# Kernel tuning notes

Measured on AMD Instinct MI355X. Metric: run time of the kernel, lower is better.

Reference implementation:

```python
import jax, jax.numpy as jnp
import numpy as np

B, L, E, H = 2, 2048, 1024, 16
HD = E // H          # head_dim = 64
G = H // 4           # heads per kernel-size group = 4


def _dwconv(x, w, b):
    """Causal depthwise conv. x: (B, G, L, D); w: (D, k); b: (D,).
    Matches PadLeft(k-1) + Conv1d(D, D, k, groups=D): y[l] = sum_j w[:, j] * x[l - (k-1) + j] + b."""
    k = w.shape[-1]
    Lx = x.shape[2]
    xp = jnp.pad(x, ((0, 0), (0, 0), (k - 1, 0), (0, 0)))
    out = b
    for j in range(k):
        out = out + xp[:, :, j:j + Lx, :] * w[:, j]
    return out


def setup_inputs() -> dict:
    key = jax.random.key(0)
    ks = jax.random.split(key, 32)
    s = 0.02
    inp = {"x": jax.random.normal(ks[0], (B, L, E), jnp.float32)}
    for i, n in enumerate(["Wq", "Wk", "Wv", "Wo"]):
        inp[n] = jax.random.normal(ks[1 + i], (E, E), jnp.float32) * s
    inp["bo"] = jax.random.normal(ks[5], (E,), jnp.float32) * s
    i = 6
    for ksz in (3, 5, 7):
        for pfx in ("q", "k", "v"):
            inp[f"{pfx}{ksz}_w"] = jax.random.normal(ks[i], (HD, ksz), jnp.float32) * (1.0 / ksz)
            inp[f"{pfx}{ksz}_b"] = jax.random.normal(ks[i + 1], (HD,), jnp.float32) * s
            i += 2
    return inp


def reference(x, Wq, Wk, Wv, Wo, bo,
              q3_w, q3_b, k3_w, k3_b, v3_w, v3_b,
              q5_w, q5_b, k5_w, k5_b, v5_w, v5_b,
              q7_w, q7_b, k7_w, k7_b, v7_w, v7_b):
    b, l, _ = x.shape

    def split(t):  # (b, l, E) -> (b, 4, G, l, HD)
        return t.reshape(b, l, 4, G, HD).transpose(0, 2, 3, 1, 4)

    q = split(x @ Wq.T)
    k = split(x @ Wk.T)
    v = split(x @ Wv.T)

    # NOTE: faithful to source quirks -- k and v convs are applied to the
    # (already convolved) q group, not to k/v.
    q0, k0, v0 = q[:, 0], k[:, 0], v[:, 0]
    q1 = _dwconv(q[:, 1], q3_w, q3_b)
    k1 = _dwconv(q1, k3_w, k3_b)
    v1 = _dwconv(q1, v3_w, v3_b)
    q2 = _dwconv(q[:, 2], q5_w, q5_b)
    k2 = _dwconv(q2, k5_w, k5_b)
    v2 = _dwconv(q2, v5_w, v5_b)
    q3 = _dwconv(q[:, 3], q7_w, q7_b)
    k3 = _dwconv(q3, k7_w, k7_b)
    v3 = _dwconv(q3, v7_w, v7_b)

    Q = jnp.concatenate([q0, q1, q2, q3], axis=1)  # (b, H, l, HD)
    K = jnp.concatenate([k0, k1, k2, k3], axis=1)
    V = jnp.concatenate([v0, v1, v2, v3], axis=1)

    logit = jnp.einsum('bnid,bnjd->bnij', Q, K) * (HD ** -0.5)
    attn = jax.nn.softmax(logit, axis=-1)
    attn_out = jnp.einsum('bnij,bnjd->bnid', attn, V)

    # Source quirk: output uses rearranged V, discarding attn_out.
    out = V.transpose(0, 2, 1, 3).reshape(b, l, E)
    # keep the attention compute alive without changing the math
    out = out + 0.0 * attn_out.transpose(0, 2, 1, 3).reshape(b, l, E)
    return out @ Wo.T + bo
```

## Files before the change

kernel.cpp:

```cpp
#include <hip/hip_runtime.h>
#include <hip/hip_bf16.h>
#include <stdint.h>

#define L_SEQ 2048
#define MTOT  4096
#define EDIM  1024

typedef __attribute__((ext_vector_type(8))) short bf16x8;
typedef __attribute__((ext_vector_type(4))) float f32x4;
typedef __attribute__((ext_vector_type(4))) float float4v;
typedef __attribute__((ext_vector_type(4))) unsigned short us4;

__device__ __forceinline__ unsigned short f2b(float f) {
    union { float f; unsigned u; } v; v.f = f;
    return (unsigned short)((v.u + 0x7FFFu + ((v.u >> 16) & 1u)) >> 16);
}
__device__ __forceinline__ float b2f(unsigned short h) {
    union { unsigned u; float f; } v; v.u = ((unsigned)h) << 16;
    return v.f;
}
__device__ __forceinline__ unsigned cvtpk(float lo, float hi) {
    unsigned r;
    asm("v_cvt_pk_bf16_f32 %0, %1, %2" : "=v"(r) : "v"(lo), "v"(hi));
    return r;
}

__device__ __forceinline__ void lds16(const void* g, void* l) {
    __builtin_amdgcn_global_load_lds((const __attribute__((address_space(1))) void*)g,
                                     (__attribute__((address_space(3))) void*)l, 16, 0, 0);
}

__global__ __launch_bounds__(256) void wprep_kernel(
    const float* __restrict__ Wq, const float* __restrict__ Wv,
    const float* __restrict__ Wo,
    unsigned short* __restrict__ W1b, unsigned short* __restrict__ Wob,
    const float* __restrict__ q3w, const float* __restrict__ q3b,
    const float* __restrict__ v3w, const float* __restrict__ v3b,
    const float* __restrict__ q5w, const float* __restrict__ q5b,
    const float* __restrict__ v5w, const float* __restrict__ v5b,
    const float* __restrict__ q7w, const float* __restrict__ q7b,
    const float* __restrict__ v7w, const float* __restrict__ v7b,
    float* __restrict__ H, float* __restrict__ Beff, float* __restrict__ Corr)
{
    if (blockIdx.x >= 2048) {
        int ch = (blockIdx.x - 2048) * 256 + threadIdx.x;
        int g = ch >> 8;
        int d = ch & 63;
        int k = 3 + 2 * g;
        const float* qw = (g == 0) ? q3w : (g == 1) ? q5w : q7w;
        const float* qb = (g == 0) ? q3b : (g == 1) ? q5b : q7b;
        const float* vw = (g == 0) ? v3w : (g == 1) ? v5w : v7w;
        const float* vb = (g == 0) ? v3b : (g == 1) ? v5b : v7b;

        float hq[7], hv[7];
        for (int i = 0; i < 7; ++i) { hq[i] = 0.f; hv[i] = 0.f; }
        for (int i = 0; i < k; ++i) {
            hq[i] = qw[d * k + (k - 1 - i)];
            hv[i] = vw[d * k + (k - 1 - i)];
        }
        float h[13];
        for (int i = 0; i < 13; ++i) h[i] = 0.f;
        for (int a = 0; a < 7; ++a)
            for (int b = 0; b < 7; ++b)
                h[a + b] += hq[a] * hv[b];
        for (int i = 0; i < 13; ++i) H[i * 768 + ch] = h[i];

        float sv = 0.f;
        for (int j = 0; j < k; ++j) sv += vw[d * k + j];
        Beff[ch] = qb[d] * sv + vb[d];

        for (int l = 0; l < 6; ++l) {
            float s2 = 0.f;
            for (int i = l + 1; i < 7; ++i) s2 += hv[i];
            Corr[l * 768 + ch] = qb[d] * s2;
        }
        return;
    }
    const int WQ = (EDIM * EDIM) / 4;
    int i = blockIdx.x * 256 + threadIdx.x;
    const float* src;
    unsigned short* dst;
    int j;
    if (i < WQ) {
        j = i * 4;
        int row = j >> 10;
        src = (row < 256) ? Wv : Wq;
        dst = W1b;
    } else {
        j = (i - WQ) * 4; src = Wo; dst = Wob;
    }
    float4v v = *(const float4v*)(src + j);
    us4 o;
    o[0] = f2b(v[0]); o[1] = f2b(v[1]); o[2] = f2b(v[2]); o[3] = f2b(v[3]);
    *(us4*)(dst + j) = o;
}

template <int TA, int OUT_MODE>
__global__ __launch_bounds__(512, 2) void gemm_f(
    const float* __restrict__ Af,
    const unsigned short* __restrict__ Ab0, const unsigned short* __restrict__ Ab1,
    int tsplit,
    const unsigned short* __restrict__ BT,
    unsigned short* __restrict__ Cb, float* __restrict__ Cf,
    const float* __restrict__ bias)
{
    constexpr int ABUF = TA ? 49152 : 32768;
    constexpr int ABYT = TA ? 32768 : 16384;
    __shared__ uint8_t sh[3 * ABUF];

    int orig = blockIdx.y * 8 + blockIdx.x;
    int wg   = (orig & 7) * 32 + (orig >> 3);
    const int m0 = (wg >> 3) * 128, n0 = (wg & 7) * 128;

    const int tid  = threadIdx.x;
    const int wid  = tid >> 6;
    const int lane = tid & 63;
    const int wr   = wid >> 2;
    const int wc   = (wid >> 1) & 1;
    const int kh   = wid & 1;
    const int fr   = lane & 15, fq = lane >> 4;

    f32x4 acc[4][4] = {};

    auto stage = [&](int buf, int t) {
        uint8_t* Abase = sh + buf * ABUF;
        uint8_t* Bbase = Abase + ABYT;
        if (TA) {
            const float* Asrc = Af + (size_t)m0 * EDIM + t * 64;
#pragma unroll
            for (int j = 0; j < 4; ++j) {
                int slot = j * 512 + tid;
                int row = slot >> 4, c = (slot & 15) ^ (row & 15);
                lds16(Asrc + (size_t)row * EDIM + c * 4,
                      Abase + j * 8192 + wid * 1024);
            }
        } else {
            const unsigned short* Asrc =
                (t < tsplit ? Ab0 : Ab1) + (size_t)m0 * EDIM + t * 64;
#pragma unroll
            for (int j = 0; j < 2; ++j) {
                int slot = j * 512 + tid;
                int row = slot >> 3, c = (slot & 7) ^ (row & 7);
                lds16(Asrc + (size_t)row * EDIM + c * 8,
                      Abase + j * 8192 + wid * 1024);
            }
        }
        const unsigned short* Bsrc = BT + (size_t)n0 * EDIM + t * 64;
#pragma unroll
        for (int j = 0; j < 2; ++j) {
            int slot = j * 512 + tid;
            int row = slot >> 3, c = (slot & 7) ^ (row & 7);
            lds16(Bsrc + (size_t)row * EDIM + c * 8,
                  Bbase + j * 8192 + wid * 1024);
        }
    };

    auto compute = [&](int buf) {
        const uint8_t* Abase = sh + buf * ABUF;
        const unsigned short* bs = (const unsigned short*)(Abase + ABYT);
        bf16x8 a[4], b[4];
#pragma unroll
        for (int mi = 0; mi < 4; ++mi) {
            int row = wr * 64 + mi * 16 + fr;
            if (TA) {
                const float* as = (const float*)Abase;
                int c0 = kh * 8 + fq * 2;
                f32x4 lo = *(const f32x4*)(as + row * 64 + ((c0 ^ (row & 15)) * 4));
                f32x4 hi = *(const f32x4*)(as + row * 64 + (((c0 + 1) ^ (row & 15)) * 4));
                union { unsigned u[4]; bf16x8 v; } fu;
                fu.u[0] = cvtpk(lo[0], lo[1]); fu.u[1] = cvtpk(lo[2], lo[3]);
                fu.u[2] = cvtpk(hi[0], hi[1]); fu.u[3] = cvtpk(hi[2], hi[3]);
                a[mi] = fu.v;
            } else {
                const unsigned short* as = (const unsigned short*)Abase;
                a[mi] = *(const bf16x8*)(as + row * 64 + (((kh * 4 + fq) ^ (row & 7)) * 8));
            }
        }
#pragma unroll
        for (int ni = 0; ni < 4; ++ni) {
            int row = wc * 64 + ni * 16 + fr;
            b[ni] = *(const bf16x8*)(bs + row * 64 + (((kh * 4 + fq) ^ (row & 7)) * 8));
        }
#pragma unroll
        for (int mi = 0; mi < 4; ++mi)
#pragma unroll
            for (int ni = 0; ni < 4; ++ni)
                acc[mi][ni] = __builtin_amdgcn_mfma_f32_16x16x32_bf16(a[mi], b[ni], acc[mi][ni], 0, 0, 0);
    };

    const int NT = EDIM >> 6;
    stage(0, 0);
    stage(1, 1);
    if (TA) asm volatile("s_waitcnt vmcnt(6)" ::: "memory");
    else    asm volatile("s_waitcnt vmcnt(4)" ::: "memory");
    __builtin_amdgcn_s_barrier();
    asm volatile("" ::: "memory");

    for (int t = 0; t < NT; ++t) {
        if (t + 2 < NT) stage((t + 2) % 3, t + 2);
        compute(t % 3);
        if (t + 1 < NT) {
            if (t + 2 < NT) {
                if (TA) asm volatile("s_waitcnt vmcnt(6)" ::: "memory");
                else    asm volatile("s_waitcnt vmcnt(4)" ::: "memory");
            } else {
                asm volatile("s_waitcnt vmcnt(0)" ::: "memory");
            }
            __builtin_amdgcn_s_barrier();
            asm volatile("" ::: "memory");
        }
    }

    __syncthreads();
    float* Mg = (float*)sh;
    const int mgbase = (wr * 2 + wc) * 4096;
    if (kh) {
#pragma unroll
        for (int mi = 0; mi < 4; ++mi)
#pragma unroll
            for (int ni = 0; ni < 4; ++ni) {
                int col = ni * 16 + fr;
                int adr = mgbase + col * 64 + (((mi * 4 + fq) ^ (col & 15)) << 2);
                *(f32x4*)(Mg + adr) = acc[mi][ni];
            }
    }
    __syncthreads();
    if (!kh) {
#pragma unroll
        for (int mi = 0; mi < 4; ++mi) {
#pragma unroll
            for (int ni = 0; ni < 4; ++ni) {
                int col = ni * 16 + fr;
                int adr = mgbase + col * 64 + (((mi * 4 + fq) ^ (col & 15)) << 2);
                f32x4 p = *(const f32x4*)(Mg + adr);
                int gcol = n0 + wc * 64 + col;
                int rowb = m0 + wr * 64 + mi * 16 + fq * 4;
#pragma unroll
                for (int j = 0; j < 4; ++j) {
                    float v = acc[mi][ni][j] + p[j];
                    if (OUT_MODE == 0) {
                        Cb[(size_t)(rowb + j) * EDIM + gcol] = f2b(v);
                    } else {
                        Cf[(size_t)(rowb + j) * EDIM + gcol] = v + bias[gcol];
                    }
                }
            }
        }
    }
}

__global__ __launch_bounds__(256) void conv_kernel(
    const unsigned short* __restrict__ T, unsigned short* __restrict__ V,
    const float* __restrict__ H, const float* __restrict__ Beff,
    const float* __restrict__ Corr)
{
    unsigned w  = blockIdx.x * 256 + threadIdx.x;
    unsigned rp = w / 192u;
    int c4 = (int)(w - rp * 192u);
    int m  = (int)rp * 2;
    int ch = c4 * 4;
    int e0 = 256 + ch;
    const unsigned short* tp = T + (size_t)m * EDIM + e0;
    unsigned short*       vp = V + (size_t)m * EDIM + e0;
    int l  = m & (L_SEQ - 1);
    float4v b4 = *(const float4v*)(Beff + ch);
    float4v acc0 = b4, acc1 = b4;

    {
        float4v h = *(const float4v*)(H + ch);
        us4 t = *(const us4*)(tp + EDIM);
        acc1[0] += h[0] * b2f(t[0]); acc1[1] += h[1] * b2f(t[1]);
        acc1[2] += h[2] * b2f(t[2]); acc1[3] += h[3] * b2f(t[3]);
    }
    int ni = (l < 12) ? l : 12;
    for (int i = 0; i <= ni; ++i) {
        us4 t = *(const us4*)(tp - (size_t)i * EDIM);
        float4v h0 = *(const float4v*)(H + i * 768 + ch);
        acc0[0] += h0[0] * b2f(t[0]); acc0[1] += h0[1] * b2f(t[1]);
        acc0[2] += h0[2] * b2f(t[2]); acc0[3] += h0[3] * b2f(t[3]);
        if (i < 12) {
            float4v h1 = *(const float4v*)(H + (i + 1) * 768 + ch);
            acc1[0] += h1[0] * b2f(t[0]); acc1[1] += h1[1] * b2f(t[1]);
            acc1[2] += h1[2] * b2f(t[2]); acc1[3] += h1[3] * b2f(t[3]);
        }
    }
    if (l < 6) {
        float4v c = *(const float4v*)(Corr + l * 768 + ch);
        acc0[0] -= c[0]; acc0[1] -= c[1]; acc0[2] -= c[2]; acc0[3] -= c[3];
    }
    if (l + 1 < 6) {
        float4v c = *(const float4v*)(Corr + (l + 1) * 768 + ch);
        acc1[0] -= c[0]; acc1[1] -= c[1]; acc1[2] -= c[2]; acc1[3] -= c[3];
    }
    us4 o0, o1;
    o0[0] = f2b(acc0[0]); o0[1] = f2b(acc0[1]); o0[2] = f2b(acc0[2]); o0[3] = f2b(acc0[3]);
    o1[0] = f2b(acc1[0]); o1[1] = f2b(acc1[1]); o1[2] = f2b(acc1[2]); o1[3] = f2b(acc1[3]);
    *(us4*)vp = o0;
    *(us4*)(vp + EDIM) = o1;
}

extern "C" void kernel_launch(void* const* d_in, const int* in_sizes, int n_in,
                              void* d_out, int out_size, void* d_ws, size_t ws_size,
                              hipStream_t stream)
{
    const float* x  = (const float*)d_in[0];
    const float* Wq = (const float*)d_in[1];
    const float* Wv = (const float*)d_in[3];
    const float* Wo = (const float*)d_in[4];
    const float* bo = (const float*)d_in[5];

    uint8_t* ws = (uint8_t*)d_ws;
    unsigned short* W1b = (unsigned short*)(ws);
    unsigned short* Wob = (unsigned short*)(ws + (2u  << 20));
    unsigned short* T   = (unsigned short*)(ws + (4u  << 20));
    unsigned short* V   = (unsigned short*)(ws + (12u << 20));
    float* H    = (float*)(ws + (20u << 20));
    float* Beff = (float*)(ws + (20u << 20) + (64u << 10));
    float* Corr = (float*)(ws + (20u << 20) + (96u << 10));

    wprep_kernel<<<2051, 256, 0, stream>>>(
        Wq, Wv, Wo, W1b, Wob,
        (const float*)d_in[6],  (const float*)d_in[7],
        (const float*)d_in[10], (const float*)d_in[11],
        (const float*)d_in[12], (const float*)d_in[13],
        (const float*)d_in[16], (const float*)d_in[17],
        (const float*)d_in[18], (const float*)d_in[19],
        (const float*)d_in[22], (const float*)d_in[23],
        H, Beff, Corr);

    dim3 gg(EDIM / 128, MTOT / 128);
    gemm_f<1, 0><<<gg, 512, 0, stream>>>(x, nullptr, nullptr, 0,
                                         W1b, T, nullptr, nullptr);

    conv_kernel<<<1536, 256, 0, stream>>>(T, V, H, Beff, Corr);

    gemm_f<0, 1><<<gg, 512, 0, stream>>>(nullptr, T, V, 4,
                                         Wob, nullptr, (float*)d_out, bo);
}
```

Before: 53.42 us.

## Fuse weight prep, two GEMMs and conv into one persistent kernel with grid barriers

Replaces four separate kernel launches with a single 256-block persistent kernel. It runs weight conversion, the first GEMM, the depthwise conv and the output GEMM in sequence, separated by a software grid barrier built from hierarchical atomic counters. The aim is to remove launch gaps and tail effects between stages. The risks are spin-wait barrier cost, a shared memory size fixed at the larger GEMM's needs (which can limit occupancy), an extra memset for the barrier state, and a dependence on all 256 blocks being co-resident.

New measurement: 147.3 us. 2.76x slower.

```diff
diff --git a/kernel.cpp b/kernel.cpp
--- a/kernel.cpp
+++ b/kernel.cpp
@@ -24,79 +24,42 @@
     asm("v_cvt_pk_bf16_f32 %0, %1, %2" : "=v"(r) : "v"(lo), "v"(hi));
     return r;
 }
-
 __device__ __forceinline__ void lds16(const void* g, void* l) {
     __builtin_amdgcn_global_load_lds((const __attribute__((address_space(1))) void*)g,
                                      (__attribute__((address_space(3))) void*)l, 16, 0, 0);
 }
 
-__global__ __launch_bounds__(256) void wprep_kernel(
-    const float* __restrict__ Wq, const float* __restrict__ Wv,
-    const float* __restrict__ Wo,
-    unsigned short* __restrict__ W1b, unsigned short* __restrict__ Wob,
-    const float* __restrict__ q3w, const float* __restrict__ q3b,
-    const float* __restrict__ v3w, const float* __restrict__ v3b,
-    const float* __restrict__ q5w, const float* __restrict__ q5b,
-    const float* __restrict__ v5w, const float* __restrict__ v5b,
-    const float* __restrict__ q7w, const float* __restrict__ q7b,
-    const float* __restrict__ v7w, const float* __restrict__ v7b,
-    float* __restrict__ H, float* __restrict__ Beff, float* __restrict__ Corr)
-{
-    if (blockIdx.x >= 2048) {
-        int ch = (blockIdx.x - 2048) * 256 + threadIdx.x;
-        int g = ch >> 8;
-        int d = ch & 63;
-        int k = 3 + 2 * g;
-        const float* qw = (g == 0) ? q3w : (g == 1) ? q5w : q7w;
-        const float* qb = (g == 0) ? q3b : (g == 1) ? q5b : q7b;
-        const float* vw = (g == 0) ? v3w : (g == 1) ? v5w : v7w;
-        const float* vb = (g == 0) ? v3b : (g == 1) ? v5b : v7b;
-
-        float hq[7], hv[7];
-        for (int i = 0; i < 7; ++i) { hq[i] = 0.f; hv[i] = 0.f; }
-        for (int i = 0; i < k; ++i) {
-            hq[i] = qw[d * k + (k - 1 - i)];
-            hv[i] = vw[d * k + (k - 1 - i)];
-        }
-        float h[13];
-        for (int i = 0; i < 13; ++i) h[i] = 0.f;
-        for (int a = 0; a < 7; ++a)
-            for (int b = 0; b < 7; ++b)
-                h[a + b] += hq[a] * hv[b];
-        for (int i = 0; i < 13; ++i) H[i * 768 + ch] = h[i];
-
-        float sv = 0.f;
-        for (int j = 0; j < k; ++j) sv += vw[d * k + j];
-        Beff[ch] = qb[d] * sv + vb[d];
-
-        for (int l = 0; l < 6; ++l) {
-            float s2 = 0.f;
-            for (int i = l + 1; i < 7; ++i) s2 += hv[i];
-            Corr[l * 768 + ch] = qb[d] * s2;
-        }
-        return;
-    }
-    const int WQ = (EDIM * EDIM) / 4;
-    int i = blockIdx.x * 256 + threadIdx.x;
-    const float* src;
-    unsigned short* dst;
-    int j;
-    if (i < WQ) {
-        j = i * 4;
-        int row = j >> 10;
-        src = (row < 256) ? Wv : Wq;
-        dst = W1b;
-    } else {
-        j = (i - WQ) * 4; src = Wo; dst = Wob;
-    }
-    float4v v = *(const float4v*)(src + j);
-    us4 o;
-    o[0] = f2b(v[0]); o[1] = f2b(v[1]); o[2] = f2b(v[2]); o[3] = f2b(v[3]);
-    *(us4*)(dst + j) = o;
+__device__ __forceinline__ void gridbar(unsigned* st) {
+    __syncthreads();
+    if (threadIdx.x == 0) {
+        __threadfence();
+        unsigned* gcnt = st + (blockIdx.x & 7) * 16;
+        unsigned* mid  = st + 128;
+        unsigned* gen  = st + 129;
+        unsigned g0 = __hip_atomic_load(gen, __ATOMIC_RELAXED, __HIP_MEMORY_SCOPE_AGENT);
+        unsigned a  = __hip_atomic_fetch_add(gcnt, 1u, __ATOMIC_ACQ_REL, __HIP_MEMORY_SCOPE_AGENT);
+        bool done = false;
+        if (a == 31u) {
+            unsigned m = __hip_atomic_fetch_add(mid, 1u, __ATOMIC_ACQ_REL, __HIP_MEMORY_SCOPE_AGENT);
+            if (m == 7u) {
+                for (int i = 0; i < 8; ++i)
+                    __hip_atomic_store(st + i * 16, 0u, __ATOMIC_RELAXED, __HIP_MEMORY_SCOPE_AGENT);
+                __hip_atomic_store(mid, 0u, __ATOMIC_RELAXED, __HIP_MEMORY_SCOPE_AGENT);
+                __hip_atomic_fetch_add(gen, 1u, __ATOMIC_RELEASE, __HIP_MEMORY_SCOPE_AGENT);
+                done = true;
+            }
+        }
+        if (!done) {
+            while (__hip_atomic_load(gen, __ATOMIC_ACQUIRE, __HIP_MEMORY_SCOPE_AGENT) == g0)
+                __builtin_amdgcn_s_sleep(4);
+        }
+    }
+    __syncthreads();
 }
 
 template <int TA, int OUT_MODE>
-__global__ __launch_bounds__(512, 2) void gemm_f(
+__device__ __forceinline__ void gemm_phase(
+    uint8_t* sh, int blk,
     const float* __restrict__ Af,
     const unsigned short* __restrict__ Ab0, const unsigned short* __restrict__ Ab1,
     int tsplit,
@@ -106,10 +69,8 @@
 {
     constexpr int ABUF = TA ? 49152 : 32768;
     constexpr int ABYT = TA ? 32768 : 16384;
-    __shared__ uint8_t sh[3 * ABUF];
-
-    int orig = blockIdx.y * 8 + blockIdx.x;
-    int wg   = (orig & 7) * 32 + (orig >> 3);
+
+    int wg = (blk & 7) * 32 + (blk >> 3);
     const int m0 = (wg >> 3) * 128, n0 = (wg & 7) * 128;
 
     const int tid  = threadIdx.x;
@@ -247,56 +208,124 @@
             }
         }
     }
-}
-
-__global__ __launch_bounds__(256) void conv_kernel(
-    const unsigned short* __restrict__ T, unsigned short* __restrict__ V,
-    const float* __restrict__ H, const float* __restrict__ Beff,
-    const float* __restrict__ Corr)
+    __syncthreads();
+}
+
+__global__ __launch_bounds__(512, 2) void mega_kernel(
+    const float* __restrict__ x, const float* __restrict__ Wq,
+    const float* __restrict__ Wv, const float* __restrict__ Wo,
+    const float* __restrict__ bo,
+    const float* __restrict__ q3w, const float* __restrict__ q3b,
+    const float* __restrict__ v3w, const float* __restrict__ v3b,
+    const float* __restrict__ q5w, const float* __restrict__ q5b,
+    const float* __restrict__ v5w, const float* __restrict__ v5b,
+    const float* __restrict__ q7w, const float* __restrict__ q7b,
+    const float* __restrict__ v7w, const float* __restrict__ v7b,
+    unsigned short* __restrict__ W1b, unsigned short* __restrict__ Wob,
+    unsigned short* __restrict__ T, unsigned short* __restrict__ V,
+    float* __restrict__ H, float* __restrict__ Beff, float* __restrict__ Corr,
+    unsigned* __restrict__ bar, float* __restrict__ out)
 {
-    unsigned w  = blockIdx.x * 256 + threadIdx.x;
-    unsigned rp = w / 192u;
-    int c4 = (int)(w - rp * 192u);
-    int m  = (int)rp * 2;
-    int ch = c4 * 4;
-    int e0 = 256 + ch;
-    const unsigned short* tp = T + (size_t)m * EDIM + e0;
-    unsigned short*       vp = V + (size_t)m * EDIM + e0;
-    int l  = m & (L_SEQ - 1);
-    float4v b4 = *(const float4v*)(Beff + ch);
-    float4v acc0 = b4, acc1 = b4;
-
-    {
-        float4v h = *(const float4v*)(H + ch);
-        us4 t = *(const us4*)(tp + EDIM);
-        acc1[0] += h[0] * b2f(t[0]); acc1[1] += h[1] * b2f(t[1]);
-        acc1[2] += h[2] * b2f(t[2]); acc1[3] += h[3] * b2f(t[3]);
-    }
-    int ni = (l < 12) ? l : 12;
-    for (int i = 0; i <= ni; ++i) {
-        us4 t = *(const us4*)(tp - (size_t)i * EDIM);
-        float4v h0 = *(const float4v*)(H + i * 768 + ch);
-        acc0[0] += h0[0] * b2f(t[0]); acc0[1] += h0[1] * b2f(t[1]);
-        acc0[2] += h0[2] * b2f(t[2]); acc0[3] += h0[3] * b2f(t[3]);
-        if (i < 12) {
-            float4v h1 = *(const float4v*)(H + (i + 1) * 768 + ch);
-            acc1[0] += h1[0] * b2f(t[0]); acc1[1] += h1[1] * b2f(t[1]);
-            acc1[2] += h1[2] * b2f(t[2]); acc1[3] += h1[3] * b2f(t[3]);
-        }
-    }
-    if (l < 6) {
-        float4v c = *(const float4v*)(Corr + l * 768 + ch);
-        acc0[0] -= c[0]; acc0[1] -= c[1]; acc0[2] -= c[2]; acc0[3] -= c[3];
-    }
-    if (l + 1 < 6) {
-        float4v c = *(const float4v*)(Corr + (l + 1) * 768 + ch);
-        acc1[0] -= c[0]; acc1[1] -= c[1]; acc1[2] -= c[2]; acc1[3] -= c[3];
-    }
-    us4 o0, o1;
-    o0[0] = f2b(acc0[0]); o0[1] = f2b(acc0[1]); o0[2] = f2b(acc0[2]); o0[3] = f2b(acc0[3]);
-    o1[0] = f2b(acc1[0]); o1[1] = f2b(acc1[1]); o1[2] = f2b(acc1[2]); o1[3] = f2b(acc1[3]);
-    *(us4*)vp = o0;
-    *(us4*)(vp + EDIM) = o1;
+    __shared__ uint8_t sh[3 * 49152];
+    const int gtid = blockIdx.x * 512 + threadIdx.x;
+
+#pragma unroll
+    for (int r = 0; r < 2; ++r) {
+        int j = (gtid * 2 + r) * 4;
+        int row = j >> 10;
+        const float* s1 = (row < 256) ? Wv : Wq;
+        float4v v1 = *(const float4v*)(s1 + j);
+        us4 o1;
+        o1[0] = f2b(v1[0]); o1[1] = f2b(v1[1]); o1[2] = f2b(v1[2]); o1[3] = f2b(v1[3]);
+        *(us4*)(W1b + j) = o1;
+        float4v v2 = *(const float4v*)(Wo + j);
+        us4 o2;
+        o2[0] = f2b(v2[0]); o2[1] = f2b(v2[1]); o2[2] = f2b(v2[2]); o2[3] = f2b(v2[3]);
+        *(us4*)(Wob + j) = o2;
+    }
+    if (gtid < 768) {
+        int ch = gtid;
+        int g = ch >> 8, d = ch & 63, k = 3 + 2 * g;
+        const float* qw = (g == 0) ? q3w : (g == 1) ? q5w : q7w;
+        const float* qb = (g == 0) ? q3b : (g == 1) ? q5b : q7b;
+        const float* vw = (g == 0) ? v3w : (g == 1) ? v5w : v7w;
+        const float* vb = (g == 0) ? v3b : (g == 1) ? v5b : v7b;
+        float hq[7], hv[7];
+        for (int i = 0; i < 7; ++i) { hq[i] = 0.f; hv[i] = 0.f; }
+        for (int i = 0; i < k; ++i) {
+            hq[i] = qw[d * k + (k - 1 - i)];
+            hv[i] = vw[d * k + (k - 1 - i)];
+        }
+        float h[13];
+        for (int i = 0; i < 13; ++i) h[i] = 0.f;
+        for (int a = 0; a < 7; ++a)
+            for (int b = 0; b < 7; ++b)
+                h[a + b] += hq[a] * hv[b];
+        for (int i = 0; i < 13; ++i) H[i * 768 + ch] = h[i];
+        float sv = 0.f;
+        for (int j = 0; j < k; ++j) sv += vw[d * k + j];
+        Beff[ch] = qb[d] * sv + vb[d];
+        for (int l = 0; l < 6; ++l) {
+            float s2 = 0.f;
+            for (int i = l + 1; i < 7; ++i) s2 += hv[i];
+            Corr[l * 768 + ch] = qb[d] * s2;
+        }
+    }
+    gridbar(bar);
+
+    gemm_phase<1, 0>(sh, blockIdx.x, x, nullptr, nullptr, 0,
+                     W1b, T, nullptr, nullptr);
+    gridbar(bar);
+
+#pragma unroll
+    for (int it = 0; it < 3; ++it) {
+        unsigned w = (unsigned)it * 131072u + (unsigned)gtid;
+        unsigned rp = w / 192u;
+        int c4 = (int)(w - rp * 192u);
+        int m  = (int)rp * 2;
+        int ch = c4 * 4;
+        int e0 = 256 + ch;
+        const unsigned short* tp = T + (size_t)m * EDIM + e0;
+        unsigned short*       vp = V + (size_t)m * EDIM + e0;
+        int l = m & (L_SEQ - 1);
+        float4v b4 = *(const float4v*)(Beff + ch);
+        float4v acc0 = b4, acc1 = b4;
+        {
+            float4v h = *(const float4v*)(H + ch);
+            us4 t = *(const us4*)(tp + EDIM);
+            acc1[0] += h[0] * b2f(t[0]); acc1[1] += h[1] * b2f(t[1]);
+            acc1[2] += h[2] * b2f(t[2]); acc1[3] += h[3] * b2f(t[3]);
+        }
+        int ni = (l < 12) ? l : 12;
+        for (int i = 0; i <= ni; ++i) {
+            us4 t = *(const us4*)(tp - (size_t)i * EDIM);
+            float4v h0 = *(const float4v*)(H + i * 768 + ch);
+            acc0[0] += h0[0] * b2f(t[0]); acc0[1] += h0[1] * b2f(t[1]);
+            acc0[2] += h0[2] * b2f(t[2]); acc0[3] += h0[3] * b2f(t[3]);
+            if (i < 12) {
+                float4v h1 = *(const float4v*)(H + (i + 1) * 768 + ch);
+                acc1[0] += h1[0] * b2f(t[0]); acc1[1] += h1[1] * b2f(t[1]);
+                acc1[2] += h1[2] * b2f(t[2]); acc1[3] += h1[3] * b2f(t[3]);
+            }
+        }
+        if (l < 6) {
+            float4v c = *(const float4v*)(Corr + l * 768 + ch);
+            acc0[0] -= c[0]; acc0[1] -= c[1]; acc0[2] -= c[2]; acc0[3] -= c[3];
+        }
+        if (l + 1 < 6) {
+            float4v c = *(const float4v*)(Corr + (l + 1) * 768 + ch);
+            acc1[0] -= c[0]; acc1[1] -= c[1]; acc1[2] -= c[2]; acc1[3] -= c[3];
+        }
+        us4 o0, o1;
+        o0[0] = f2b(acc0[0]); o0[1] = f2b(acc0[1]); o0[2] = f2b(acc0[2]); o0[3] = f2b(acc0[3]);
+        o1[0] = f2b(acc1[0]); o1[1] = f2b(acc1[1]); o1[2] = f2b(acc1[2]); o1[3] = f2b(acc1[3]);
+        *(us4*)vp = o0;
+        *(us4*)(vp + EDIM) = o1;
+    }
+    gridbar(bar);
+
+    gemm_phase<0, 1>(sh, blockIdx.x, nullptr, T, V, 4,
+                     Wob, nullptr, out, bo);
 }
 
 extern "C" void kernel_launch(void* const* d_in, const int* in_sizes, int n_in,
@@ -317,23 +346,17 @@
     float* H    = (float*)(ws + (20u << 20));
     float* Beff = (float*)(ws + (20u << 20) + (64u << 10));
     float* Corr = (float*)(ws + (20u << 20) + (96u << 10));
-
-    wprep_kernel<<<2051, 256, 0, stream>>>(
-        Wq, Wv, Wo, W1b, Wob,
+    unsigned* bar = (unsigned*)(ws + (21u << 20));
+
+    hipMemsetAsync(bar, 0, 1024, stream);
+
+    mega_kernel<<<256, 512, 0, stream>>>(
+        x, Wq, Wv, Wo, bo,
         (const float*)d_in[6],  (const float*)d_in[7],
         (const float*)d_in[10], (const float*)d_in[11],
         (const float*)d_in[12], (const float*)d_in[13],
         (const float*)d_in[16], (const float*)d_in[17],
         (const float*)d_in[18], (const float*)d_in[19],
         (const float*)d_in[22], (const float*)d_in[23],
-        H, Beff, Corr);
-
-    dim3 gg(EDIM / 128, MTOT / 128);
-    gemm_f<1, 0><<<gg, 512, 0, stream>>>(x, nullptr, nullptr, 0,
-                                         W1b, T, nullptr, nullptr);
-
-    conv_kernel<<<1536, 256, 0, stream>>>(T, V, H, Beff, Corr);
-
-    gemm_f<0, 1><<<gg, 512, 0, stream>>>(nullptr, T, V, 4,
-                                         Wob, nullptr, (float*)d_out, bo);
-}
+        W1b, Wob, T, V, H, Beff, Corr, bar, (float*)d_out);
+}
```

## Replace 128x128 split-K GEMM tiles with 64x64 tiles and no K-split merge

Applied to the files above, without the earlier changes.

Both GEMMs now use 64x64 output tiles with 256 threads and four waves, each wave owning a 32x32 quadrant over the full K range. This replaces 128x128 tiles where wave pairs split K and merged partial sums through LDS. The first GEMM's fp32 A operand uses a K step of 32 to keep the LDS footprint small. The goal is more blocks (1024 instead of 256) across the CUs, higher occupancy, and no reduction epilogue, at the cost of less operand reuse per tile and more global and L2 traffic.

Measured after the change: 60.02 us. 1.12x slower.

```diff
diff --git a/kernel.cpp b/kernel.cpp
--- a/kernel.cpp
+++ b/kernel.cpp
@@ -24,7 +24,6 @@
     asm("v_cvt_pk_bf16_f32 %0, %1, %2" : "=v"(r) : "v"(lo), "v"(hi));
     return r;
 }
-
 __device__ __forceinline__ void lds16(const void* g, void* l) {
     __builtin_amdgcn_global_load_lds((const __attribute__((address_space(1))) void*)g,
                                      (__attribute__((address_space(3))) void*)l, 16, 0, 0);
@@ -44,9 +43,7 @@
 {
     if (blockIdx.x >= 2048) {
         int ch = (blockIdx.x - 2048) * 256 + threadIdx.x;
-        int g = ch >> 8;
-        int d = ch & 63;
-        int k = 3 + 2 * g;
+        int g = ch >> 8, d = ch & 63, k = 3 + 2 * g;
         const float* qw = (g == 0) ? q3w : (g == 1) ? q5w : q7w;
         const float* qb = (g == 0) ? q3b : (g == 1) ? q5b : q7b;
         const float* vw = (g == 0) ? v3w : (g == 1) ? v5w : v7w;
@@ -96,7 +93,7 @@
 }
 
 template <int TA, int OUT_MODE>
-__global__ __launch_bounds__(512, 2) void gemm_f(
+__global__ __launch_bounds__(256, TA ? 4 : 3) void gemm64(
     const float* __restrict__ Af,
     const unsigned short* __restrict__ Ab0, const unsigned short* __restrict__ Ab1,
     int tsplit,
@@ -104,94 +101,118 @@
     unsigned short* __restrict__ Cb, float* __restrict__ Cf,
     const float* __restrict__ bias)
 {
-    constexpr int ABUF = TA ? 49152 : 32768;
-    constexpr int ABYT = TA ? 32768 : 16384;
-    __shared__ uint8_t sh[3 * ABUF];
-
-    int orig = blockIdx.y * 8 + blockIdx.x;
-    int wg   = (orig & 7) * 32 + (orig >> 3);
-    const int m0 = (wg >> 3) * 128, n0 = (wg & 7) * 128;
+    constexpr int BK   = TA ? 32 : 64;
+    constexpr int NT   = 1024 / BK;
+    constexpr int ABYT = 8192;
+    constexpr int BBYT = TA ? 4096 : 8192;
+    constexpr int BUF  = ABYT + BBYT;
+    __shared__ uint8_t sh[3 * BUF];
+
+    int orig = blockIdx.y * 16 + blockIdx.x;
+    int wg   = (orig & 7) * 128 + (orig >> 3);
+    const int m0 = (wg >> 4) * 64, n0 = (wg & 15) * 64;
 
     const int tid  = threadIdx.x;
     const int wid  = tid >> 6;
     const int lane = tid & 63;
-    const int wr   = wid >> 2;
-    const int wc   = (wid >> 1) & 1;
-    const int kh   = wid & 1;
+    const int wr   = wid >> 1, wc = wid & 1;
     const int fr   = lane & 15, fq = lane >> 4;
 
-    f32x4 acc[4][4] = {};
+    f32x4 acc[2][2] = {};
 
     auto stage = [&](int buf, int t) {
-        uint8_t* Abase = sh + buf * ABUF;
+        uint8_t* Abase = sh + buf * BUF;
         uint8_t* Bbase = Abase + ABYT;
         if (TA) {
-            const float* Asrc = Af + (size_t)m0 * EDIM + t * 64;
-#pragma unroll
-            for (int j = 0; j < 4; ++j) {
-                int slot = j * 512 + tid;
-                int row = slot >> 4, c = (slot & 15) ^ (row & 15);
+            const float* Asrc = Af + (size_t)m0 * EDIM + t * 32;
+#pragma unroll
+            for (int j = 0; j < 2; ++j) {
+                int slot = j * 256 + tid;
+                int row = slot >> 3, c = (slot & 7) ^ (row & 7);
                 lds16(Asrc + (size_t)row * EDIM + c * 4,
-                      Abase + j * 8192 + wid * 1024);
+                      Abase + j * 4096 + wid * 1024);
+            }
+            const unsigned short* Bsrc = BT + (size_t)n0 * EDIM + t * 32;
+            {
+                int row = tid >> 2, c = (tid & 3) ^ (row & 3);
+                lds16(Bsrc + (size_t)row * EDIM + c * 8, Bbase + wid * 1024);
             }
         } else {
             const unsigned short* Asrc =
                 (t < tsplit ? Ab0 : Ab1) + (size_t)m0 * EDIM + t * 64;
 #pragma unroll
             for (int j = 0; j < 2; ++j) {
-                int slot = j * 512 + tid;
+                int slot = j * 256 + tid;
                 int row = slot >> 3, c = (slot & 7) ^ (row & 7);
                 lds16(Asrc + (size_t)row * EDIM + c * 8,
-                      Abase + j * 8192 + wid * 1024);
-            }
-        }
-        const unsigned short* Bsrc = BT + (size_t)n0 * EDIM + t * 64;
-#pragma unroll
-        for (int j = 0; j < 2; ++j) {
-            int slot = j * 512 + tid;
-            int row = slot >> 3, c = (slot & 7) ^ (row & 7);
-            lds16(Bsrc + (size_t)row * EDIM + c * 8,
-                  Bbase + j * 8192 + wid * 1024);
+                      Abase + j * 4096 + wid * 1024);
+            }
+            const unsigned short* Bsrc = BT + (size_t)n0 * EDIM + t * 64;
+#pragma unroll
+            for (int j = 0; j < 2; ++j) {
+                int slot = j * 256 + tid;
+                int row = slot >> 3, c = (slot & 7) ^ (row & 7);
+                lds16(Bsrc + (size_t)row * EDIM + c * 8,
+                      Bbase + j * 4096 + wid * 1024);
+            }
         }
     };
 
     auto compute = [&](int buf) {
-        const uint8_t* Abase = sh + buf * ABUF;
-        const unsigned short* bs = (const unsigned short*)(Abase + ABYT);
-        bf16x8 a[4], b[4];
-#pragma unroll
-        for (int mi = 0; mi < 4; ++mi) {
-            int row = wr * 64 + mi * 16 + fr;
-            if (TA) {
-                const float* as = (const float*)Abase;
-                int c0 = kh * 8 + fq * 2;
-                f32x4 lo = *(const f32x4*)(as + row * 64 + ((c0 ^ (row & 15)) * 4));
-                f32x4 hi = *(const f32x4*)(as + row * 64 + (((c0 + 1) ^ (row & 15)) * 4));
+        const uint8_t* Abase = sh + buf * BUF;
+        if (TA) {
+            const float* as = (const float*)Abase;
+            const unsigned short* bs = (const unsigned short*)(Abase + ABYT);
+            bf16x8 a[2], b[2];
+#pragma unroll
+            for (int mi = 0; mi < 2; ++mi) {
+                int row = wr * 32 + mi * 16 + fr;
+                int c0 = fq * 2;
+                f32x4 lo = *(const f32x4*)(as + row * 32 + ((c0 ^ (row & 7)) * 4));
+                f32x4 hi = *(const f32x4*)(as + row * 32 + (((c0 + 1) ^ (row & 7)) * 4));
                 union { unsigned u[4]; bf16x8 v; } fu;
                 fu.u[0] = cvtpk(lo[0], lo[1]); fu.u[1] = cvtpk(lo[2], lo[3]);
                 fu.u[2] = cvtpk(hi[0], hi[1]); fu.u[3] = cvtpk(hi[2], hi[3]);
                 a[mi] = fu.v;
-            } else {
-                const unsigned short* as = (const unsigned short*)Abase;
-                a[mi] = *(const bf16x8*)(as + row * 64 + (((kh * 4 + fq) ^ (row & 7)) * 8));
-            }
-        }
-#pragma unroll
-        for (int ni = 0; ni < 4; ++ni) {
-            int row = wc * 64 + ni * 16 + fr;
-            b[ni] = *(const bf16x8*)(bs + row * 64 + (((kh * 4 + fq) ^ (row & 7)) * 8));
-        }
-#pragma unroll
-        for (int mi = 0; mi < 4; ++mi)
-#pragma unroll
-            for (int ni = 0; ni < 4; ++ni)
-                acc[mi][ni] = __builtin_amdgcn_mfma_f32_16x16x32_bf16(a[mi], b[ni], acc[mi][ni], 0, 0, 0);
+            }
+#pragma unroll
+            for (int ni = 0; ni < 2; ++ni) {
+                int row = wc * 32 + ni * 16 + fr;
+                b[ni] = *(const bf16x8*)(bs + row * 32 + (((fq) ^ (row & 3)) * 8));
+            }
+#pragma unroll
+            for (int mi = 0; mi < 2; ++mi)
+#pragma unroll
+                for (int ni = 0; ni < 2; ++ni)
+                    acc[mi][ni] = __builtin_amdgcn_mfma_f32_16x16x32_bf16(a[mi], b[ni], acc[mi][ni], 0, 0, 0);
+        } else {
+            const unsigned short* as = (const unsigned short*)Abase;
+            const unsigned short* bs = (const unsigned short*)(Abase + ABYT);
+#pragma unroll
+            for (int s = 0; s < 2; ++s) {
+                bf16x8 a[2], b[2];
+#pragma unroll
+                for (int mi = 0; mi < 2; ++mi) {
+                    int row = wr * 32 + mi * 16 + fr;
+                    a[mi] = *(const bf16x8*)(as + row * 64 + (((s * 4 + fq) ^ (row & 7)) * 8));
+                }
+#pragma unroll
+                for (int ni = 0; ni < 2; ++ni) {
+                    int row = wc * 32 + ni * 16 + fr;
+                    b[ni] = *(const bf16x8*)(bs + row * 64 + (((s * 4 + fq) ^ (row & 7)) * 8));
+                }
+#pragma unroll
+                for (int mi = 0; mi < 2; ++mi)
+#pragma unroll
+                    for (int ni = 0; ni < 2; ++ni)
+                        acc[mi][ni] = __builtin_amdgcn_mfma_f32_16x16x32_bf16(a[mi], b[ni], acc[mi][ni], 0, 0, 0);
+            }
+        }
     };
 
-    const int NT = EDIM >> 6;
     stage(0, 0);
     stage(1, 1);
-    if (TA) asm volatile("s_waitcnt vmcnt(6)" ::: "memory");
+    if (TA) asm volatile("s_waitcnt vmcnt(3)" ::: "memory");
     else    asm volatile("s_waitcnt vmcnt(4)" ::: "memory");
     __builtin_amdgcn_s_barrier();
     asm volatile("" ::: "memory");
@@ -201,7 +222,7 @@
         compute(t % 3);
         if (t + 1 < NT) {
             if (t + 2 < NT) {
-                if (TA) asm volatile("s_waitcnt vmcnt(6)" ::: "memory");
+                if (TA) asm volatile("s_waitcnt vmcnt(3)" ::: "memory");
                 else    asm volatile("s_waitcnt vmcnt(4)" ::: "memory");
             } else {
                 asm volatile("s_waitcnt vmcnt(0)" ::: "memory");
@@ -211,38 +232,19 @@
         }
     }
 
-    __syncthreads();
-    float* Mg = (float*)sh;
-    const int mgbase = (wr * 2 + wc) * 4096;
-    if (kh) {
-#pragma unroll
-        for (int mi = 0; mi < 4; ++mi)
-#pragma unroll
-            for (int ni = 0; ni < 4; ++ni) {
-                int col = ni * 16 + fr;
-                int adr = mgbase + col * 64 + (((mi * 4 + fq) ^ (col & 15)) << 2);
-                *(f32x4*)(Mg + adr) = acc[mi][ni];
-            }
-    }
-    __syncthreads();
-    if (!kh) {
-#pragma unroll
-        for (int mi = 0; mi < 4; ++mi) {
-#pragma unroll
-            for (int ni = 0; ni < 4; ++ni) {
-                int col = ni * 16 + fr;
-                int adr = mgbase + col * 64 + (((mi * 4 + fq) ^ (col & 15)) << 2);
-                f32x4 p = *(const f32x4*)(Mg + adr);
-                int gcol = n0 + wc * 64 + col;
-                int rowb = m0 + wr * 64 + mi * 16 + fq * 4;
-#pragma unroll
-                for (int j = 0; j < 4; ++j) {
-                    float v = acc[mi][ni][j] + p[j];
-                    if (OUT_MODE == 0) {
-                        Cb[(size_t)(rowb + j) * EDIM + gcol] = f2b(v);
-                    } else {
-                        Cf[(size_t)(rowb + j) * EDIM + gcol] = v + bias[gcol];
-                    }
+#pragma unroll
+    for (int mi = 0; mi < 2; ++mi) {
+#pragma unroll
+        for (int ni = 0; ni < 2; ++ni) {
+            int col  = n0 + wc * 32 + ni * 16 + fr;
+            int rowb = m0 + wr * 32 + mi * 16 + fq * 4;
+#pragma unroll
+            for (int j = 0; j < 4; ++j) {
+                float v = acc[mi][ni][j];
+                if (OUT_MODE == 0) {
+                    Cb[(size_t)(rowb + j) * EDIM + col] = f2b(v);
+                } else {
+                    Cf[(size_t)(rowb + j) * EDIM + col] = v + bias[col];
                 }
             }
         }
@@ -328,12 +330,12 @@
         (const float*)d_in[22], (const float*)d_in[23],
         H, Beff, Corr);
 
-    dim3 gg(EDIM / 128, MTOT / 128);
-    gemm_f<1, 0><<<gg, 512, 0, stream>>>(x, nullptr, nullptr, 0,
+    dim3 gg(EDIM / 64, MTOT / 64);
+    gemm64<1, 0><<<gg, 256, 0, stream>>>(x, nullptr, nullptr, 0,
                                          W1b, T, nullptr, nullptr);
 
     conv_kernel<<<1536, 256, 0, stream>>>(T, V, H, Beff, Corr);
 
-    gemm_f<0, 1><<<gg, 512, 0, stream>>>(nullptr, T, V, 4,
+    gemm64<0, 1><<<gg, 256, 0, stream>>>(nullptr, T, V, 4,
                                          Wob, nullptr, (float*)d_out, bo);
 }
```
